# Kernel tuning notes

Hardware: AMD Instinct MI355X
Metric: run time of the kernel (lower is better)

Reference implementation:

```python
import jax, jax.numpy as jnp
import numpy as np

H = 16  # num_heads

def setup_inputs() -> dict:
    key = jax.random.key(0)
    ks = jax.random.split(key, 9)
    B, S, E = 2, 2048, 1024
    d = E // H  # 64, shared KV head dim
    sc = lambda n: 1.0 / np.sqrt(n)
    return {
        "x": jax.random.normal(ks[0], (B, S, E), jnp.float32),
        "wq": jax.random.normal(ks[1], (E, E), jnp.float32) * sc(E),
        "bq": jax.random.normal(ks[2], (E,), jnp.float32) * 0.02,
        "wk": jax.random.normal(ks[3], (E, d), jnp.float32) * sc(E),
        "bk": jax.random.normal(ks[4], (d,), jnp.float32) * 0.02,
        "wv": jax.random.normal(ks[5], (E, d), jnp.float32) * sc(E),
        "bv": jax.random.normal(ks[6], (d,), jnp.float32) * 0.02,
        "wo": jax.random.normal(ks[7], (E, E), jnp.float32) * sc(E),
        "bo": jax.random.normal(ks[8], (E,), jnp.float32) * 0.02,
    }

def reference(x, wq, bq, wk, bk, wv, bv, wo, bo):
    B, S, E = x.shape
    d = E // H
    Q = (x @ wq + bq).reshape(B, S, H, d).transpose(0, 2, 1, 3)  # [B,H,S,d]
    K = x @ wk + bk  # [B,S,d] shared across heads (MQA)
    V = x @ wv + bv  # [B,S,d]
    scores = jnp.einsum('bhqd,bkd->bhqk', Q, K) / np.sqrt(d)  # [B,H,S,S]
    weights = jax.nn.softmax(scores, axis=-1)
    attn = jnp.einsum('bhqk,bkd->bhqd', weights, V)  # [B,H,S,d]
    # FAITHFUL to source: reshape [B,H,S,d] -> [B,S,E] WITHOUT permuting back
    attn = attn.reshape(B, S, E)
    return attn @ wo + bo
```

## Files before the change

kernel.cpp:

```cpp
#include <hip/hip_runtime.h>
#include <hip/hip_bf16.h>

#define BB 2
#define SS 2048
#define EE 1024
#define HH 16
#define DD 64

using bfrag  = __attribute__((ext_vector_type(8))) short;
using bfrag4 = __attribute__((ext_vector_type(4))) short;
using ffrag  = __attribute__((ext_vector_type(4))) float;
using uint2v = __attribute__((ext_vector_type(2))) uint;

#define MFMA32(A, B, C) __builtin_amdgcn_mfma_f32_16x16x32_bf16(A, B, C, 0, 0, 0)
#define MFMA16(A, B, C) __builtin_amdgcn_mfma_f32_16x16x16bf16_1k(A, B, C, 0, 0, 0)

static __device__ __forceinline__ ushort f2bf(float f) {
  __hip_bfloat16 h = __float2bfloat16(f);
  return *reinterpret_cast<ushort*>(&h);
}

static __device__ __forceinline__ uint pack_bf2(float lo, float hi) {
  uint a = __float_as_uint(lo) + 0x8000u;
  uint b = __float_as_uint(hi) + 0x8000u;
  return __builtin_amdgcn_perm(b, a, 0x07060302u);
}

static __device__ __forceinline__ void gl_lds16(const ushort* g, ushort* l) {
  __builtin_amdgcn_global_load_lds(
      (const __attribute__((address_space(1))) void*)g,
      (__attribute__((address_space(3))) void*)l, 16, 0, 0);
}

__global__ __launch_bounds__(256) void prep(
    const float* __restrict__ x, const float* __restrict__ wq,
    const float* __restrict__ wk, const float* __restrict__ wv,
    const float* __restrict__ wo, ushort* __restrict__ xb,
    ushort* __restrict__ wqkvT, ushort* __restrict__ woT) {
  __shared__ float t[32][33];
  int id = blockIdx.x;
  if (id < 4096) {
    int i = id * 256 + threadIdx.x;
    float4 v = ((const float4*)x)[i];
    ushort4 u = { f2bf(v.x), f2bf(v.y), f2bf(v.z), f2bf(v.w) };
    ((ushort4*)xb)[i] = u;
    return;
  }
  id -= 4096;
  const float* src;
  ushort* dst;
  int N, bx, by;
  if (id < 1024)      { src = wq; dst = wqkvT;                      N = 1024; bx = id & 31;          by = id >> 5; }
  else if (id < 2048) { src = wo; dst = woT;                        N = 1024; bx = (id - 1024) & 31; by = (id - 1024) >> 5; }
  else if (id < 2112) { src = wk; dst = wqkvT + (size_t)1024 * 1024; N = 64;  bx = (id - 2048) & 1;  by = (id - 2048) >> 1; }
  else                { src = wv; dst = wqkvT + (size_t)1088 * 1024; N = 64;  bx = (id - 2112) & 1;  by = (id - 2112) >> 1; }
  const int k0 = by * 32, n0 = bx * 32;
  const int tx = threadIdx.x & 31, ty = threadIdx.x >> 5;
  #pragma unroll
  for (int i = 0; i < 32; i += 8)
    t[ty + i][tx] = src[(size_t)(k0 + ty + i) * N + n0 + tx];
  __syncthreads();
  #pragma unroll
  for (int i = 0; i < 32; i += 8)
    dst[(size_t)(n0 + ty + i) * 1024 + k0 + tx] = f2bf(t[tx][ty + i]);
}

template <bool QKV>
__global__ __launch_bounds__(256) void gemm_mfma3(
    const ushort* __restrict__ A, const ushort* __restrict__ Bt,
    const float* __restrict__ bias0, const float* __restrict__ bias1,
    const float* __restrict__ bias2, void* __restrict__ O1,
    ushort* __restrict__ Kb, ushort* __restrict__ VTb,
    int M, int N, int K, float qscale) {
  __shared__ __align__(16) ushort As[2][128 * 64];
  __shared__ __align__(16) ushort Bs[2][64 * 64];
  const int tid = threadIdx.x;
  const int lane = tid & 63;
  const int quad = lane >> 4;
  const int c = lane & 15;
  const int wv = tid >> 6;
  const int wm = (wv & 1) * 64;
  const int wn = (wv >> 1) * 32;
  const size_t m0 = (size_t)blockIdx.y * 128;
  const size_t n0 = (size_t)blockIdx.x * 64;

  const int srow = lane >> 3;
  const int sck = (lane & 7) ^ srow;

  ffrag zero = {0.f, 0.f, 0.f, 0.f};
  ffrag acc[4][2];
  #pragma unroll
  for (int mt = 0; mt < 4; ++mt)
    #pragma unroll
    for (int nt = 0; nt < 2; ++nt) acc[mt][nt] = zero;

  const int NK = K >> 6;
  #pragma unroll
  for (int i = 0; i < 4; ++i) {
    int ia = wv * 4 + i;
    gl_lds16(&A[(m0 + ia * 8 + srow) * (size_t)K + sck * 8], &As[0][ia * 512]);
  }
  #pragma unroll
  for (int i = 0; i < 2; ++i) {
    int ib = wv * 2 + i;
    gl_lds16(&Bt[(n0 + ib * 8 + srow) * (size_t)K + sck * 8], &Bs[0][ib * 512]);
  }
  __syncthreads();

  for (int ki = 0; ki < NK; ++ki) {
    const int buf = ki & 1;
    if (ki + 1 < NK) {
      int k0 = (ki + 1) << 6;
      #pragma unroll
      for (int i = 0; i < 4; ++i) {
        int ia = wv * 4 + i;
        gl_lds16(&A[(m0 + ia * 8 + srow) * (size_t)K + k0 + sck * 8],
                 &As[buf ^ 1][ia * 512]);
      }
      #pragma unroll
      for (int i = 0; i < 2; ++i) {
        int ib = wv * 2 + i;
        gl_lds16(&Bt[(n0 + ib * 8 + srow) * (size_t)K + k0 + sck * 8],
                 &Bs[buf ^ 1][ib * 512]);
      }
    }
    #pragma unroll
    for (int ks = 0; ks < 2; ++ks) {
      bfrag af[4], bf[2];
      #pragma unroll
      for (int mt = 0; mt < 4; ++mt) {
        int ra = wm + mt * 16 + c;
        af[mt] = *(const bfrag*)&As[buf][(ra * 8 + ((ks * 4 + quad) ^ (ra & 7))) * 8];
      }
      #pragma unroll
      for (int nt = 0; nt < 2; ++nt) {
        int rb = wn + nt * 16 + c;
        bf[nt] = *(const bfrag*)&Bs[buf][(rb * 8 + ((ks * 4 + quad) ^ (rb & 7))) * 8];
      }
      #pragma unroll
      for (int mt = 0; mt < 4; ++mt)
        #pragma unroll
        for (int nt = 0; nt < 2; ++nt)
          acc[mt][nt] = MFMA32(af[mt], bf[nt], acc[mt][nt]);
    }
    __syncthreads();
  }

  #pragma unroll
  for (int nt = 0; nt < 2; ++nt) {
    const int colb = (int)n0 + wn + nt * 16;
    if (QKV) {
      if (colb < 1024) {
        float bb = bias0[colb + c];
        ushort* dst = (ushort*)O1 + colb;
        #pragma unroll
        for (int mt = 0; mt < 4; ++mt)
          #pragma unroll
          for (int r = 0; r < 4; ++r) {
            size_t row = m0 + wm + mt * 16 + quad * 4 + r;
            dst[row * 1024 + c] = f2bf((acc[mt][nt][r] + bb) * qscale);
          }
      } else if (colb < 1088) {
        float bb = bias1[colb - 1024 + c];
        ushort* dst = Kb + (colb - 1024);
        #pragma unroll
        for (int mt = 0; mt < 4; ++mt)
          #pragma unroll
          for (int r = 0; r < 4; ++r) {
            size_t row = m0 + wm + mt * 16 + quad * 4 + r;
            dst[row * 64 + c] = f2bf(acc[mt][nt][r] + bb);
          }
      } else {
        int d = colb - 1088 + c;
        float bb = bias2[colb - 1088 + c];
        int bidx = (int)(m0 >> 11);
        ushort* dstv = VTb + ((size_t)(bidx * 64 + d)) * SS;
        #pragma unroll
        for (int mt = 0; mt < 4; ++mt) {
          int sb = (int)(m0 & 2047) + wm + mt * 16 + quad * 4;
          uint2v u;
          u.x = pack_bf2(acc[mt][nt][0] + bb, acc[mt][nt][1] + bb);
          u.y = pack_bf2(acc[mt][nt][2] + bb, acc[mt][nt][3] + bb);
          *(uint2v*)&dstv[sb] = u;
        }
      }
    } else {
      float bb = bias0[colb + c];
      float* dst = (float*)O1;
      #pragma unroll
      for (int mt = 0; mt < 4; ++mt)
        #pragma unroll
        for (int r = 0; r < 4; ++r) {
          size_t row = m0 + wm + mt * 16 + quad * 4 + r;
          dst[row * (size_t)N + colb + c] = acc[mt][nt][r] + bb;
        }
    }
  }
}

__global__ __launch_bounds__(512) void mqa_attn10(
    const ushort* __restrict__ Q, const ushort* __restrict__ Kg,
    const ushort* __restrict__ VT, ushort* __restrict__ A2) {
  __shared__ __align__(16) ushort Kt[2][2][4096];
  __shared__ __align__(16) ushort Vt[2][2][4096];
  const int tid = threadIdx.x;
  const int lane = tid & 63;
  const int quad = lane >> 4;
  const int c = lane & 15;
  const int wv = tid >> 6;
  const int half = wv >> 2;
  const int lw = wv & 3;
  const int bid = blockIdx.x;
  const int b = bid >> 8;
  const int r = bid & 255;
  const int h = r >> 4;
  const int s0 = (r & 15) << 7;

  const int srow = lane >> 3;
  const int sck = (lane & 7) ^ srow;

  ffrag zero = {0.f, 0.f, 0.f, 0.f};
  bfrag4 ones4;
  #pragma unroll
  for (int i = 0; i < 4; ++i) ones4[i] = (short)16256;

  bfrag aq[2][2];
  #pragma unroll
  for (int mt = 0; mt < 2; ++mt) {
    const ushort* qp =
        Q + ((size_t)(b * SS) + s0 + lw * 32 + mt * 16 + c) * EE + h * 64 + quad * 8;
    aq[mt][0] = *(const bfrag*)qp;
    aq[mt][1] = *(const bfrag*)(qp + 32);
  }

  ffrag o[2][4];
  #pragma unroll
  for (int mt = 0; mt < 2; ++mt)
    #pragma unroll
    for (int nt = 0; nt < 4; ++nt) o[mt][nt] = zero;
  ffrag ls[2] = {zero, zero};

  const int koff = half << 10;
  const ushort* Kbase = Kg + (size_t)b * SS * 64;
  const ushort* Vbase = VT + (size_t)b * 64 * SS;
  const int i0 = lw * 2, i1 = lw * 2 + 1;
  const int r0 = i0 * 8 + srow, r1 = i1 * 8 + srow;

  gl_lds16(Kbase + (size_t)(koff + r0) * 64 + sck * 8, &Kt[half][0][i0 * 512]);
  gl_lds16(Kbase + (size_t)(koff + r1) * 64 + sck * 8, &Kt[half][0][i1 * 512]);
  gl_lds16(Vbase + (size_t)r0 * SS + koff + sck * 8, &Vt[half][0][i0 * 512]);
  gl_lds16(Vbase + (size_t)r1 * SS + koff + sck * 8, &Vt[half][0][i1 * 512]);
  __syncthreads();

  for (int it = 0; it < 16; ++it) {
    const int buf = it & 1;
    if (it + 1 < 16) {
      int kb = koff + ((it + 1) << 6);
      gl_lds16(Kbase + (size_t)(kb + r0) * 64 + sck * 8, &Kt[half][buf ^ 1][i0 * 512]);
      gl_lds16(Kbase + (size_t)(kb + r1) * 64 + sck * 8, &Kt[half][buf ^ 1][i1 * 512]);
      gl_lds16(Vbase + (size_t)r0 * SS + kb + sck * 8, &Vt[half][buf ^ 1][i0 * 512]);
      gl_lds16(Vbase + (size_t)r1 * SS + kb + sck * 8, &Vt[half][buf ^ 1][i1 * 512]);
    }

    #pragma unroll
    for (int kt = 0; kt < 4; ++kt) {
      const int key = kt * 16 + c;
      const int k7 = key & 7;
      bfrag kf0 = *(const bfrag*)&Kt[half][buf][(key * 8 + (quad ^ k7)) * 8];
      bfrag kf1 = *(const bfrag*)&Kt[half][buf][(key * 8 + ((quad + 4) ^ k7)) * 8];
      bfrag4 pb[2];
      #pragma unroll
      for (int mt = 0; mt < 2; ++mt) {
        ffrag st = MFMA32(kf0, aq[mt][0], zero);
        st = MFMA32(kf1, aq[mt][1], st);
        uint2v uu;
        uu.x = pack_bf2(__builtin_amdgcn_exp2f(st[0]),
                        __builtin_amdgcn_exp2f(st[1]));
        uu.y = pack_bf2(__builtin_amdgcn_exp2f(st[2]),
                        __builtin_amdgcn_exp2f(st[3]));
        pb[mt] = __builtin_bit_cast(bfrag4, uu);
      }
      const int ck = kt * 2 + (quad >> 1);
      const int wc = (quad & 1) * 4;
      #pragma unroll
      for (int nt = 0; nt < 4; ++nt) {
        int d = nt * 16 + c;
        bfrag4 vf = *(const bfrag4*)&Vt[half][buf][(d * 8 + (ck ^ (d & 7))) * 8 + wc];
        #pragma unroll
        for (int mt = 0; mt < 2; ++mt)
          o[mt][nt] = MFMA16(vf, pb[mt], o[mt][nt]);
      }
      #pragma unroll
      for (int mt = 0; mt < 2; ++mt)
        ls[mt] = MFMA16(ones4, pb[mt], ls[mt]);
    }
    __syncthreads();
  }

  float* cbuf = (float*)&Kt[0][0][0];
  float* lbuf = (float*)&Vt[0][0][0];
  if (half == 1) {
    float* wb = cbuf + (size_t)lw * 2048;
    #pragma unroll
    for (int mt = 0; mt < 2; ++mt) {
      #pragma unroll
      for (int nt = 0; nt < 4; ++nt)
        *(ffrag*)&wb[(mt * 4 + nt) * 256 + lane * 4] = o[mt][nt];
      lbuf[lw * 128 + mt * 64 + lane] = ls[mt][0];
    }
  }
  __syncthreads();
  if (half == 1) return;

  const float* rb = cbuf + (size_t)lw * 2048;
  #pragma unroll
  for (int mt = 0; mt < 2; ++mt) {
    #pragma unroll
    for (int nt = 0; nt < 4; ++nt) {
      ffrag p = *(const ffrag*)&rb[(mt * 4 + nt) * 256 + lane * 4];
      o[mt][nt] += p;
    }
    const float inv = 1.f / (ls[mt][0] + lbuf[lw * 128 + mt * 64 + lane]);
    const int sp = h * 128 + (s0 >> 4) + lw * 2 + mt;
    ushort* orow = A2 + ((size_t)b * SS + sp) * EE;
    #pragma unroll
    for (int nt = 0; nt < 4; ++nt) {
      uint2v u;
      u.x = pack_bf2(o[mt][nt][0] * inv, o[mt][nt][1] * inv);
      u.y = pack_bf2(o[mt][nt][2] * inv, o[mt][nt][3] * inv);
      *(uint2v*)&orow[c * 64 + nt * 16 + quad * 4] = u;
    }
  }
}

extern "C" void kernel_launch(void* const* d_in, const int* in_sizes, int n_in,
                              void* d_out, int out_size, void* d_ws, size_t ws_size,
                              hipStream_t stream) {
  const float* x  = (const float*)d_in[0];
  const float* wq = (const float*)d_in[1];
  const float* bq = (const float*)d_in[2];
  const float* wk = (const float*)d_in[3];
  const float* bk = (const float*)d_in[4];
  const float* wv = (const float*)d_in[5];
  const float* bv = (const float*)d_in[6];
  const float* wo = (const float*)d_in[7];
  const float* bo = (const float*)d_in[8];
  float* out = (float*)d_out;

  char* w = (char*)d_ws;
  ushort* xb     = (ushort*)w;  w += (size_t)4096 * 1024 * 2;
  ushort* wqkvT  = (ushort*)w;  w += (size_t)1152 * 1024 * 2;
  ushort* woT    = (ushort*)w;  w += (size_t)1024 * 1024 * 2;
  ushort* Qb     = (ushort*)w;  w += (size_t)4096 * 1024 * 2;
  ushort* Kb     = (ushort*)w;  w += (size_t)4096 * 64 * 2;
  ushort* VTb    = (ushort*)w;  w += (size_t)BB * 64 * SS * 2;
  ushort* A2     = (ushort*)w;  w += (size_t)4096 * 1024 * 2;

  prep<<<6272, 256, 0, stream>>>(x, wq, wk, wv, wo, xb, wqkvT, woT);

  const float qscale = 0.18033688011112042f;
  gemm_mfma3<true><<<dim3(18, 32), 256, 0, stream>>>(
      xb, wqkvT, bq, bk, bv, Qb, Kb, VTb, 4096, 1152, 1024, qscale);

  mqa_attn10<<<512, 512, 0, stream>>>(Qb, Kb, VTb, A2);

  gemm_mfma3<false><<<dim3(16, 32), 256, 0, stream>>>(
      A2, woT, bo, nullptr, nullptr, out, nullptr, nullptr, 4096, 1024, 1024, 1.0f);
}
```

Baseline: 169.8 us.

## Use 16x16x32 MFMA for PV via permuted V^T layout; XCD-aware GEMM block swizzle

The attention PV product and the row-sum now use the K=32 bf16 MFMA instead of two K=16 MFMAs. Two key sub-tiles of probabilities are packed into one 8-element fragment, and the QKV GEMM epilogue stores V^T with a permuted column order so the fragment lanes line up. The V tile loads into LDS change to match the new swizzled layout. Separately, both GEMMs remap block indices so that consecutive blocks on each XCD share M rows, aiming for better L2 locality; the cost is more index arithmetic and a tighter coupling between the producer layout and the consumer.

```diff
diff --git a/kernel.cpp b/kernel.cpp
--- a/kernel.cpp
+++ b/kernel.cpp
@@ -11,9 +11,9 @@
 using bfrag4 = __attribute__((ext_vector_type(4))) short;
 using ffrag  = __attribute__((ext_vector_type(4))) float;
 using uint2v = __attribute__((ext_vector_type(2))) uint;
+using uint4v = __attribute__((ext_vector_type(4))) uint;
 
 #define MFMA32(A, B, C) __builtin_amdgcn_mfma_f32_16x16x32_bf16(A, B, C, 0, 0, 0)
-#define MFMA16(A, B, C) __builtin_amdgcn_mfma_f32_16x16x16bf16_1k(A, B, C, 0, 0, 0)
 
 static __device__ __forceinline__ ushort f2bf(float f) {
   __hip_bfloat16 h = __float2bfloat16(f);
@@ -81,8 +81,15 @@
   const int wv = tid >> 6;
   const int wm = (wv & 1) * 64;
   const int wn = (wv >> 1) * 32;
-  const size_t m0 = (size_t)blockIdx.y * 128;
-  const size_t n0 = (size_t)blockIdx.x * 64;
+
+  const int gx = gridDim.x, gy = gridDim.y;
+  const int lid = blockIdx.y * gx + blockIdx.x;
+  const int xcd = lid & 7;
+  const int idx = lid >> 3;
+  const int mrow = xcd * (gy >> 3) + idx / gx;
+  const int ncol = idx % gx;
+  const size_t m0 = (size_t)mrow * 128;
+  const size_t n0 = (size_t)ncol * 64;
 
   const int srow = lane >> 3;
   const int sck = (lane & 7) ^ srow;
@@ -178,10 +185,11 @@
         #pragma unroll
         for (int mt = 0; mt < 4; ++mt) {
           int sb = (int)(m0 & 2047) + wm + mt * 16 + quad * 4;
+          int col = (sb & ~31) + ((sb >> 2) & 3) * 8 + ((sb >> 4) & 1) * 4;
           uint2v u;
           u.x = pack_bf2(acc[mt][nt][0] + bb, acc[mt][nt][1] + bb);
           u.y = pack_bf2(acc[mt][nt][2] + bb, acc[mt][nt][3] + bb);
-          *(uint2v*)&dstv[sb] = u;
+          *(uint2v*)&dstv[col] = u;
         }
       }
     } else {
@@ -198,7 +206,7 @@
   }
 }
 
-__global__ __launch_bounds__(512) void mqa_attn10(
+__global__ __launch_bounds__(512) void mqa_attn15(
     const ushort* __restrict__ Q, const ushort* __restrict__ Kg,
     const ushort* __restrict__ VT, ushort* __restrict__ A2) {
   __shared__ __align__(16) ushort Kt[2][2][4096];
@@ -220,9 +228,9 @@
   const int sck = (lane & 7) ^ srow;
 
   ffrag zero = {0.f, 0.f, 0.f, 0.f};
-  bfrag4 ones4;
-  #pragma unroll
-  for (int i = 0; i < 4; ++i) ones4[i] = (short)16256;
+  bfrag ones8;
+  #pragma unroll
+  for (int i = 0; i < 8; ++i) ones8[i] = (short)16256;
 
   bfrag aq[2][2];
   #pragma unroll
@@ -246,10 +254,15 @@
   const int i0 = lw * 2, i1 = lw * 2 + 1;
   const int r0 = i0 * 8 + srow, r1 = i1 * 8 + srow;
 
+  const int vd0 = lw * 16 + (lane >> 3);
+  const int vd1 = vd0 + 8;
+  const ushort* vsrc0 = Vbase + (size_t)vd0 * SS + (((lane & 7) ^ (vd0 & 7)) * 8);
+  const ushort* vsrc1 = Vbase + (size_t)vd1 * SS + (((lane & 7) ^ (vd1 & 7)) * 8);
+
   gl_lds16(Kbase + (size_t)(koff + r0) * 64 + sck * 8, &Kt[half][0][i0 * 512]);
   gl_lds16(Kbase + (size_t)(koff + r1) * 64 + sck * 8, &Kt[half][0][i1 * 512]);
-  gl_lds16(Vbase + (size_t)r0 * SS + koff + sck * 8, &Vt[half][0][i0 * 512]);
-  gl_lds16(Vbase + (size_t)r1 * SS + koff + sck * 8, &Vt[half][0][i1 * 512]);
+  gl_lds16(vsrc0 + koff, &Vt[half][0][(lw * 16) * 64]);
+  gl_lds16(vsrc1 + koff, &Vt[half][0][(lw * 16 + 8) * 64]);
   __syncthreads();
 
   for (int it = 0; it < 16; ++it) {
@@ -258,41 +271,47 @@
       int kb = koff + ((it + 1) << 6);
       gl_lds16(Kbase + (size_t)(kb + r0) * 64 + sck * 8, &Kt[half][buf ^ 1][i0 * 512]);
       gl_lds16(Kbase + (size_t)(kb + r1) * 64 + sck * 8, &Kt[half][buf ^ 1][i1 * 512]);
-      gl_lds16(Vbase + (size_t)r0 * SS + kb + sck * 8, &Vt[half][buf ^ 1][i0 * 512]);
-      gl_lds16(Vbase + (size_t)r1 * SS + kb + sck * 8, &Vt[half][buf ^ 1][i1 * 512]);
-    }
-
-    #pragma unroll
-    for (int kt = 0; kt < 4; ++kt) {
-      const int key = kt * 16 + c;
-      const int k7 = key & 7;
-      bfrag kf0 = *(const bfrag*)&Kt[half][buf][(key * 8 + (quad ^ k7)) * 8];
-      bfrag kf1 = *(const bfrag*)&Kt[half][buf][(key * 8 + ((quad + 4) ^ k7)) * 8];
-      bfrag4 pb[2];
+      gl_lds16(vsrc0 + kb, &Vt[half][buf ^ 1][(lw * 16) * 64]);
+      gl_lds16(vsrc1 + kb, &Vt[half][buf ^ 1][(lw * 16 + 8) * 64]);
+    }
+
+    #pragma unroll
+    for (int p = 0; p < 2; ++p) {
+      uint2v uu[2][2];
+      #pragma unroll
+      for (int a = 0; a < 2; ++a) {
+        const int key = (p * 2 + a) * 16 + c;
+        const int k7 = key & 7;
+        bfrag kf0 = *(const bfrag*)&Kt[half][buf][(key * 8 + (quad ^ k7)) * 8];
+        bfrag kf1 = *(const bfrag*)&Kt[half][buf][(key * 8 + ((quad + 4) ^ k7)) * 8];
+        #pragma unroll
+        for (int mt = 0; mt < 2; ++mt) {
+          ffrag st = MFMA32(kf0, aq[mt][0], zero);
+          st = MFMA32(kf1, aq[mt][1], st);
+          uu[a][mt].x = pack_bf2(__builtin_amdgcn_exp2f(st[0]),
+                                 __builtin_amdgcn_exp2f(st[1]));
+          uu[a][mt].y = pack_bf2(__builtin_amdgcn_exp2f(st[2]),
+                                 __builtin_amdgcn_exp2f(st[3]));
+        }
+      }
+      bfrag pb8[2];
       #pragma unroll
       for (int mt = 0; mt < 2; ++mt) {
-        ffrag st = MFMA32(kf0, aq[mt][0], zero);
-        st = MFMA32(kf1, aq[mt][1], st);
-        uint2v uu;
-        uu.x = pack_bf2(__builtin_amdgcn_exp2f(st[0]),
-                        __builtin_amdgcn_exp2f(st[1]));
-        uu.y = pack_bf2(__builtin_amdgcn_exp2f(st[2]),
-                        __builtin_amdgcn_exp2f(st[3]));
-        pb[mt] = __builtin_bit_cast(bfrag4, uu);
-      }
-      const int ck = kt * 2 + (quad >> 1);
-      const int wc = (quad & 1) * 4;
+        uint4v w = {uu[0][mt].x, uu[0][mt].y, uu[1][mt].x, uu[1][mt].y};
+        pb8[mt] = __builtin_bit_cast(bfrag, w);
+      }
+      const int ch = p * 4 + quad;
       #pragma unroll
       for (int nt = 0; nt < 4; ++nt) {
         int d = nt * 16 + c;
-        bfrag4 vf = *(const bfrag4*)&Vt[half][buf][(d * 8 + (ck ^ (d & 7))) * 8 + wc];
+        bfrag vf = *(const bfrag*)&Vt[half][buf][d * 64 + ((ch ^ (d & 7)) * 8)];
         #pragma unroll
         for (int mt = 0; mt < 2; ++mt)
-          o[mt][nt] = MFMA16(vf, pb[mt], o[mt][nt]);
+          o[mt][nt] = MFMA32(vf, pb8[mt], o[mt][nt]);
       }
       #pragma unroll
       for (int mt = 0; mt < 2; ++mt)
-        ls[mt] = MFMA16(ones4, pb[mt], ls[mt]);
+        ls[mt] = MFMA32(ones8, pb8[mt], ls[mt]);
     }
     __syncthreads();
   }
@@ -317,8 +336,8 @@
   for (int mt = 0; mt < 2; ++mt) {
     #pragma unroll
     for (int nt = 0; nt < 4; ++nt) {
-      ffrag p = *(const ffrag*)&rb[(mt * 4 + nt) * 256 + lane * 4];
-      o[mt][nt] += p;
+      ffrag pp = *(const ffrag*)&rb[(mt * 4 + nt) * 256 + lane * 4];
+      o[mt][nt] += pp;
     }
     const float inv = 1.f / (ls[mt][0] + lbuf[lw * 128 + mt * 64 + lane]);
     const int sp = h * 128 + (s0 >> 4) + lw * 2 + mt;
@@ -362,7 +381,7 @@
   gemm_mfma3<true><<<dim3(18, 32), 256, 0, stream>>>(
       xb, wqkvT, bq, bk, bv, Qb, Kb, VTb, 4096, 1152, 1024, qscale);
 
-  mqa_attn10<<<512, 512, 0, stream>>>(Qb, Kb, VTb, A2);
+  mqa_attn15<<<512, 512, 0, stream>>>(Qb, Kb, VTb, A2);
 
   gemm_mfma3<false><<<dim3(16, 32), 256, 0, stream>>>(
       A2, woT, bo, nullptr, nullptr, out, nullptr, nullptr, 4096, 1024, 1024, 1.0f);
```

Result: faster. 161.1 us (median of 2 runs) (-5.1%).
